# Optimization experiments

Measured on AMD Instinct MI355X. Metric: run time of the kernel, lower is better.

Reference implementation:

```python
import jax, jax.numpy as jnp
import numpy as np

E = 1024   # embed_dim
H = 16     # num_heads
D = E // H # head dim = 64
L = 1024   # query seq len
S = 1024   # key seq len
N = 4      # batch


def _xavier(key, shape):
    fan_in, fan_out = shape[-1], shape[0]
    if len(shape) == 3:  # attn_W [D, D, H]: torch xavier treats dims (d0, d1*h)
        fan_out, fan_in = shape[0], shape[1] * shape[2]
    scale = jnp.sqrt(6.0 / (fan_in + fan_out)).astype(jnp.float32)
    return jax.random.uniform(key, shape, jnp.float32, -scale, scale)


def setup_inputs() -> dict:
    key = jax.random.key(0)
    ks = jax.random.split(key, 8)
    return {
        "Q": jax.random.normal(ks[0], (L, N, E), jnp.float32),
        "K": jax.random.normal(ks[1], (S, N, E), jnp.float32),
        "V": jax.random.normal(ks[2], (S, N, E), jnp.float32),
        "q_w": _xavier(ks[3], (E, E)),
        "k_w": _xavier(ks[4], (E, E)),
        "v_w": _xavier(ks[5], (E, E)),
        "out_w": _xavier(ks[6], (E, E)),
        "in_bias": jnp.zeros((3, E), jnp.float32),
        "out_bias": jnp.zeros((E,), jnp.float32),
        "attn_W": _xavier(ks[7], (D, D, H)),
    }


def reference(Q, K, V, q_w, k_w, v_w, out_w, in_bias, out_bias, attn_W):
    # in-projections: [l,n,e] x [o,e] -> [l,n,o]
    Qp = jnp.einsum('lni,oi->lno', Q, q_w) + in_bias[0]
    Kp = jnp.einsum('sni,oi->sno', K, k_w) + in_bias[1]
    Vp = jnp.einsum('sni,oi->sno', V, v_w) + in_bias[2]
    # split heads as (head_dim D, num_heads H) -- matches torch .view order
    Qh = Qp.reshape(L, N, D, H)
    Kh = Kp.reshape(S, N, D, H)
    Vh = Vp.reshape(S, N, D, H)
    # 'product' attention: per-head bilinear form q^T W_k k
    scores = jnp.einsum('lnok,oik,snik->lsnk', Qh, attn_W, Kh) / jnp.sqrt(jnp.float32(E))
    W = jax.nn.softmax(scores, axis=1)          # softmax over key dim s
    # dropout p=0.0 -> identity
    O = jnp.einsum('lsnk,snik->lnik', W, Vh).reshape(L, N, E)
    out = O @ out_w + out_bias
    # attention map: sum over heads, reshape [L,S,N] -> [N,L,S] (torch .view semantics = reshape)
    Wmap = W.sum(axis=-1).reshape(-1, L, S) / H
    return out, Wmap
```

## Files before the change

kernel.cpp:

```cpp
#include <hip/hip_runtime.h>
#include <cstdint>

typedef __bf16 bf16x8 __attribute__((ext_vector_type(8)));
typedef float f32x4 __attribute__((ext_vector_type(4)));

#define GLOAD_LDS16(gptr, lptr)                                              \
  __builtin_amdgcn_global_load_lds(                                          \
      (const __attribute__((address_space(1))) void*)(gptr),                 \
      (__attribute__((address_space(3))) void*)(lptr), 16, 0, 0)

static const size_t OFF_QW2BF = 0;
static const size_t OFF_KWBF  = 524288;
static const size_t OFF_VWBF  = 1048576;
static const size_t OFF_OWTBF = 1572864;
static const size_t OFF_QB2   = 2097152;
static const size_t OFF_QWBF  = 2098176;
static const size_t OFF_KHBF  = 4195328;
static const size_t OFF_VTBF  = 6292480;
static const size_t OFF_ST    = 8389632;
static const size_t OFF_OBF   = 8520704;
static const size_t OFF_ABF   = 10617856;

__device__ inline unsigned short f2bf(float f) {
  union { float f; unsigned u; } v; v.f = f;
  const unsigned r = v.u + 0x7FFFu + ((v.u >> 16) & 1u);
  return (unsigned short)(r >> 16);
}

__global__ __launch_bounds__(256) void k_qw2(const float* __restrict__ qw,
    const float* __restrict__ attnW, const float* __restrict__ bias0,
    unsigned short* __restrict__ qw2, float* __restrict__ qb2) {
  const int b = blockIdx.x;
  const int k = b >> 6, i = b & 63;
  const int tid = threadIdx.x;
  __shared__ float aw[64];
  if (tid < 64) aw[tid] = attnW[(tid * 64 + i) * 16 + k] * 0.03125f;
  __syncthreads();
  for (int j = tid; j < 1024; j += 256) {
    float acc = 0.f;
#pragma unroll 8
    for (int o = 0; o < 64; ++o) acc = fmaf(qw[(o * 16 + k) * 1024 + j], aw[o], acc);
    qw2[(size_t)b * 1024 + j] = f2bf(acc);
  }
  if (tid == 0) {
    float acc = 0.f;
    for (int o = 0; o < 64; ++o) acc = fmaf(bias0[o * 16 + k], aw[o], acc);
    qb2[b] = acc;
  }
}

__global__ __launch_bounds__(256) void k_cvt2(const float* __restrict__ a,
    const float* __restrict__ b, unsigned short* __restrict__ oa,
    unsigned short* __restrict__ ob) {
  const int o = blockIdx.x;
  const int dst = (o & 15) * 64 + (o >> 4);
  const int j = threadIdx.x;
  const float4 va = ((const float4*)(a + (size_t)o * 1024))[j];
  ushort4 ha; ha.x = f2bf(va.x); ha.y = f2bf(va.y); ha.z = f2bf(va.z); ha.w = f2bf(va.w);
  ((ushort4*)(oa + (size_t)dst * 1024))[j] = ha;
  const float4 vb = ((const float4*)(b + (size_t)o * 1024))[j];
  ushort4 hb; hb.x = f2bf(vb.x); hb.y = f2bf(vb.y); hb.z = f2bf(vb.z); hb.w = f2bf(vb.w);
  ((ushort4*)(ob + (size_t)dst * 1024))[j] = hb;
}

__global__ __launch_bounds__(256) void k_cvtA(const float* __restrict__ Q,
    const float* __restrict__ K, const float* __restrict__ V,
    unsigned short* __restrict__ out) {
  const int b = blockIdx.x;
  const int m = b >> 10;
  const float* src = m == 0 ? Q : (m == 1 ? K : V);
  unsigned short* dst = out + (size_t)m * 4194304;
#pragma unroll
  for (int q = 0; q < 4; ++q) {
    const int idx = (b & 1023) * 1024 + q * 256 + threadIdx.x;
    const float4 v = ((const float4*)src)[idx];
    ushort4 h; h.x = f2bf(v.x); h.y = f2bf(v.y); h.z = f2bf(v.z); h.w = f2bf(v.w);
    ((ushort4*)dst)[idx] = h;
  }
}

__global__ __launch_bounds__(256) void k_tr(const float* __restrict__ w,
    unsigned short* __restrict__ wt) {
  __shared__ float t[64][65];
  const int j0 = blockIdx.y * 64, o0 = blockIdx.x * 64;
  const int tid = threadIdx.x;
  const int r = tid >> 4, c4 = tid & 15;
#pragma unroll
  for (int q = 0; q < 4; ++q) {
    const int row = r + q * 16;
    const float4 v = *(const float4*)&w[(size_t)(j0 + row) * 1024 + o0 + c4 * 4];
    t[row][c4 * 4 + 0] = v.x; t[row][c4 * 4 + 1] = v.y;
    t[row][c4 * 4 + 2] = v.z; t[row][c4 * 4 + 3] = v.w;
  }
  __syncthreads();
#pragma unroll
  for (int q = 0; q < 4; ++q) {
    const int orow = r + q * 16;
    ushort4 h;
    h.x = f2bf(t[c4 * 4 + 0][orow]); h.y = f2bf(t[c4 * 4 + 1][orow]);
    h.z = f2bf(t[c4 * 4 + 2][orow]); h.w = f2bf(t[c4 * 4 + 3][orow]);
    *(ushort4*)&wt[(size_t)(o0 + orow) * 1024 + j0 + c4 * 4] = h;
  }
}

__global__ __launch_bounds__(256) void k_gemm_in(
    const unsigned short* __restrict__ Abf, const unsigned short* __restrict__ Bq,
    const unsigned short* __restrict__ Bk, const unsigned short* __restrict__ Bv,
    const float* __restrict__ bq, const float* __restrict__ bk,
    const float* __restrict__ bv, unsigned short* __restrict__ Cq,
    unsigned short* __restrict__ Ck, unsigned short* __restrict__ Cv) {
  __shared__ unsigned short As[128 * 64];
  __shared__ unsigned short Bs[128 * 64];
  const int id = blockIdx.x;
  const int g  = (id & 7) + ((id >> 6) << 3);
  const int bx = (id >> 3) & 7;
  const int by = g & 31, bz = g >> 5;
  const unsigned short* A = Abf + (size_t)bz * 4194304;
  const unsigned short* B = bz == 0 ? Bq : (bz == 1 ? Bk : Bv);
  const float* bias       = bz == 0 ? bq : (bz == 1 ? bk : bv);
  unsigned short* C       = bz == 0 ? Cq : (bz == 1 ? Ck : Cv);
  const int m0 = by * 128, o0 = bx * 128;
  const int tid = threadIdx.x;
  const int wid = tid >> 6, lane = tid & 63;
  const int wr = wid >> 1, wc = wid & 1;
  const int lr = lane & 15, lk = lane >> 4;
  int srow[4], scol[4];
#pragma unroll
  for (int q = 0; q < 4; ++q) {
    const int idx = q * 256 + tid;
    srow[q] = idx >> 3;
    scol[q] = (((idx & 7) ^ ((idx >> 3) & 7)) << 3);
  }
  f32x4 acc[4][4];
#pragma unroll
  for (int i = 0; i < 4; ++i)
#pragma unroll
    for (int j = 0; j < 4; ++j) acc[i][j] = (f32x4){0.f, 0.f, 0.f, 0.f};

  for (int t = 0; t < 16; ++t) {
    const int kb = t * 64;
#pragma unroll
    for (int q = 0; q < 4; ++q) {
      GLOAD_LDS16(&A[(size_t)(m0 + srow[q]) * 1024 + kb + scol[q]],
                  &As[(q * 256 + tid) * 8]);
      GLOAD_LDS16(&B[(size_t)(o0 + srow[q]) * 1024 + kb + scol[q]],
                  &Bs[(q * 256 + tid) * 8]);
    }
    __syncthreads();
#pragma unroll
    for (int ph = 0; ph < 2; ++ph) {
      const int ck = ph * 4 + lk;
      bf16x8 af[4], bfr[4];
#pragma unroll
      for (int f = 0; f < 4; ++f) {
        const int ra = wr * 64 + f * 16 + lr;
        af[f] = *(const bf16x8*)&As[ra * 64 + ((ck ^ (ra & 7)) << 3)];
        const int rb = wc * 64 + f * 16 + lr;
        bfr[f] = *(const bf16x8*)&Bs[rb * 64 + ((ck ^ (rb & 7)) << 3)];
      }
#pragma unroll
      for (int i = 0; i < 4; ++i)
#pragma unroll
        for (int j = 0; j < 4; ++j)
          acc[i][j] = __builtin_amdgcn_mfma_f32_16x16x32_bf16(af[i], bfr[j], acc[i][j], 0, 0, 0);
    }
    __syncthreads();
  }
#pragma unroll
  for (int fi = 0; fi < 4; ++fi)
#pragma unroll
    for (int fj = 0; fj < 4; ++fj) {
      const int o = o0 + wc * 64 + fj * 16 + lr;
      const int kk = o >> 6, ii = o & 63;
      const float bo = bz == 0 ? bias[o] : bias[ii * 16 + kk];
#pragma unroll
      for (int t = 0; t < 4; ++t) {
        const int m = m0 + wr * 64 + fi * 16 + lk * 4 + t;
        const float v = acc[fi][fj][t] + bo;
        const int l = m >> 2, nn = m & 3;
        if (bz <= 1) {
          C[(((size_t)(nn * 16 + kk) * 1024 + l) << 6) + ii] = f2bf(v);
        } else {
          C[(((size_t)(nn * 16 + kk) * 64 + ii) << 10) + l] = f2bf(v);
        }
      }
    }
}

__global__ __launch_bounds__(256) void k_gemm_out(
    const unsigned short* __restrict__ A, const unsigned short* __restrict__ B,
    const float* __restrict__ bias, float* __restrict__ C) {
  __shared__ unsigned short As[64 * 64];
  __shared__ unsigned short Bs[128 * 64];
  const int id = blockIdx.x;
  const int g  = (id & 7) + ((id >> 6) << 3);
  const int bx = (id >> 3) & 7;
  const int m0 = g * 64, o0 = bx * 128;
  const int tid = threadIdx.x;
  const int wid = tid >> 6, lane = tid & 63;
  const int wr = wid >> 1, wc = wid & 1;
  const int lr = lane & 15, lk = lane >> 4;
  int srow[4], scol[4];
#pragma unroll
  for (int q = 0; q < 4; ++q) {
    const int idx = q * 256 + tid;
    srow[q] = idx >> 3;
    scol[q] = (((idx & 7) ^ ((idx >> 3) & 7)) << 3);
  }
  f32x4 acc[2][4];
#pragma unroll
  for (int i = 0; i < 2; ++i)
#pragma unroll
    for (int j = 0; j < 4; ++j) acc[i][j] = (f32x4){0.f, 0.f, 0.f, 0.f};

  for (int t = 0; t < 16; ++t) {
    const int kb = t * 64;
#pragma unroll
    for (int q = 0; q < 2; ++q)
      GLOAD_LDS16(&A[(size_t)(m0 + srow[q]) * 1024 + kb + scol[q]],
                  &As[(q * 256 + tid) * 8]);
#pragma unroll
    for (int q = 0; q < 4; ++q)
      GLOAD_LDS16(&B[(size_t)(o0 + srow[q]) * 1024 + kb + scol[q]],
                  &Bs[(q * 256 + tid) * 8]);
    __syncthreads();
#pragma unroll
    for (int ph = 0; ph < 2; ++ph) {
      const int ck = ph * 4 + lk;
      bf16x8 af[2], bfr[4];
#pragma unroll
      for (int f = 0; f < 2; ++f) {
        const int ra = wr * 32 + f * 16 + lr;
        af[f] = *(const bf16x8*)&As[ra * 64 + ((ck ^ (ra & 7)) << 3)];
      }
#pragma unroll
      for (int f = 0; f < 4; ++f) {
        const int rb = wc * 64 + f * 16 + lr;
        bfr[f] = *(const bf16x8*)&Bs[rb * 64 + ((ck ^ (rb & 7)) << 3)];
      }
#pragma unroll
      for (int i = 0; i < 2; ++i)
#pragma unroll
        for (int j = 0; j < 4; ++j)
          acc[i][j] = __builtin_amdgcn_mfma_f32_16x16x32_bf16(af[i], bfr[j], acc[i][j], 0, 0, 0);
    }
    __syncthreads();
  }
#pragma unroll
  for (int fi = 0; fi < 2; ++fi)
#pragma unroll
    for (int fj = 0; fj < 4; ++fj) {
      const int o = o0 + wc * 64 + fj * 16 + lr;
      const float bo = bias[o];
#pragma unroll
      for (int t = 0; t < 4; ++t) {
        const int m = m0 + wr * 32 + fi * 16 + lk * 4 + t;
        C[(size_t)m * 1024 + o] = acc[fi][fj][t] + bo;
      }
    }
}

__global__ __launch_bounds__(256) void k_flash(
    const unsigned short* __restrict__ Qbf, const unsigned short* __restrict__ Khbf,
    const unsigned short* __restrict__ Vtbf, float* __restrict__ stats,
    unsigned short* __restrict__ Obf) {
  __shared__ unsigned short Kd[2][64 * 64];
  __shared__ unsigned short Vd[2][64 * 64];
  __shared__ unsigned short Ps[4][16 * 64];
  const int ob = blockIdx.x;
  const int b = (ob & 7) * 128 + (ob >> 3);
  const int lt = b & 15, k = (b >> 4) & 15, n = b >> 8;
  const int l0 = lt * 64;
  const int tid = threadIdx.x, w = tid >> 6, lane = tid & 63;
  const int lr = lane & 15, lk = lane >> 4;
  const size_t hb = (size_t)(n * 16 + k) * 65536;
  const unsigned short* qrow = Qbf + hb + (size_t)(l0 + w * 16 + lr) * 64;
  const bf16x8 qa0 = *(const bf16x8*)(qrow + lk * 8);
  const bf16x8 qa1 = *(const bf16x8*)(qrow + 32 + lk * 8);
  const int swz = lr & 7;
  int srow[2], scol[2];
#pragma unroll
  for (int q = 0; q < 2; ++q) {
    const int idx = q * 256 + tid;
    srow[q] = idx >> 3;
    scol[q] = (((idx & 7) ^ ((idx >> 3) & 7)) << 3);
  }
  const unsigned short* Kb = Khbf + hb;
  const unsigned short* Vb = Vtbf + hb;
  int4 kreg[2], vreg[2];
#pragma unroll
  for (int q = 0; q < 2; ++q) {
    kreg[q] = *(const int4*)(Kb + (size_t)srow[q] * 64 + scol[q]);
    vreg[q] = *(const int4*)(Vb + (size_t)srow[q] * 1024 + scol[q]);
  }
#pragma unroll
  for (int q = 0; q < 2; ++q) {
    *(int4*)&Kd[0][(q * 256 + tid) * 8] = kreg[q];
    *(int4*)&Vd[0][(q * 256 + tid) * 8] = vreg[q];
  }
  float m_ = -1e30f, Z_ = 0.f;
  f32x4 oacc[4];
#pragma unroll
  for (int it = 0; it < 4; ++it) oacc[it] = (f32x4){0.f, 0.f, 0.f, 0.f};
  __syncthreads();

  for (int t0 = 0; t0 < 16; ++t0) {
    const int cur = t0 & 1;
    if (t0 < 15) {
      const int s1 = (t0 + 1) * 64;
#pragma unroll
      for (int q = 0; q < 2; ++q) {
        kreg[q] = *(const int4*)(Kb + (size_t)(s1 + srow[q]) * 64 + scol[q]);
        vreg[q] = *(const int4*)(Vb + (size_t)srow[q] * 1024 + s1 + scol[q]);
      }
    }
    f32x4 sc[4];
#pragma unroll
    for (int st = 0; st < 4; ++st) {
      const int r = st * 16 + lr;
      const bf16x8 kb0 = *(const bf16x8*)&Kd[cur][r * 64 + ((lk ^ (r & 7)) << 3)];
      const bf16x8 kb1 = *(const bf16x8*)&Kd[cur][r * 64 + (((4 + lk) ^ (r & 7)) << 3)];
      f32x4 z = (f32x4){0.f, 0.f, 0.f, 0.f};
      z = __builtin_amdgcn_mfma_f32_16x16x32_bf16(kb0, qa0, z, 0, 0, 0);
      sc[st] = __builtin_amdgcn_mfma_f32_16x16x32_bf16(kb1, qa1, z, 0, 0, 0);
    }
    float tm = fmaxf(fmaxf(fmaxf(sc[0][0], sc[0][1]), fmaxf(sc[0][2], sc[0][3])),
                     fmaxf(fmaxf(sc[1][0], sc[1][1]), fmaxf(sc[1][2], sc[1][3])));
    tm = fmaxf(tm, fmaxf(fmaxf(fmaxf(sc[2][0], sc[2][1]), fmaxf(sc[2][2], sc[2][3])),
                         fmaxf(fmaxf(sc[3][0], sc[3][1]), fmaxf(sc[3][2], sc[3][3]))));
    tm = fmaxf(tm, __shfl_xor(tm, 16));
    tm = fmaxf(tm, __shfl_xor(tm, 32));
    const float mn = fmaxf(m_, tm);
    const float fac = __expf(m_ - mn);
    m_ = mn;
    float rs = 0.f;
    float p[4][4];
#pragma unroll
    for (int st = 0; st < 4; ++st)
#pragma unroll
      for (int t = 0; t < 4; ++t) {
        p[st][t] = __expf(sc[st][t] - mn);
        rs += p[st][t];
      }
    rs += __shfl_xor(rs, 16);
    rs += __shfl_xor(rs, 32);
    Z_ = Z_ * fac + rs;
#pragma unroll
    for (int st = 0; st < 4; ++st) {
      ushort4 pk;
      pk.x = f2bf(p[st][0]); pk.y = f2bf(p[st][1]);
      pk.z = f2bf(p[st][2]); pk.w = f2bf(p[st][3]);
      const int c = (st * 4 + lk) ^ (swz << 1);
      *(ushort4*)&Ps[w][lr * 64 + c * 4] = pk;
    }
    float fr[4];
#pragma unroll
    for (int t = 0; t < 4; ++t) fr[t] = __shfl(fac, lk * 4 + t);
    const f32x4 facv = {fr[0], fr[1], fr[2], fr[3]};
    const bf16x8 pa0 = *(const bf16x8*)&Ps[w][lr * 64 + ((lk ^ swz) << 3)];
    const bf16x8 pa1 = *(const bf16x8*)&Ps[w][lr * 64 + (((4 + lk) ^ swz) << 3)];
#pragma unroll
    for (int it = 0; it < 4; ++it) {
      const int r = it * 16 + lr;
      const bf16x8 bv0 = *(const bf16x8*)&Vd[cur][r * 64 + ((lk ^ (r & 7)) << 3)];
      const bf16x8 bv1 = *(const bf16x8*)&Vd[cur][r * 64 + (((4 + lk) ^ (r & 7)) << 3)];
      f32x4 o = oacc[it] * facv;
      o = __builtin_amdgcn_mfma_f32_16x16x32_bf16(pa0, bv0, o, 0, 0, 0);
      oacc[it] = __builtin_amdgcn_mfma_f32_16x16x32_bf16(pa1, bv1, o, 0, 0, 0);
    }
    if (t0 < 15) {
#pragma unroll
      for (int q = 0; q < 2; ++q) {
        *(int4*)&Kd[cur ^ 1][(q * 256 + tid) * 8] = kreg[q];
        *(int4*)&Vd[cur ^ 1][(q * 256 + tid) * 8] = vreg[q];
      }
    }
    __syncthreads();
  }

  if (lane < 16) {
    const size_t so = ((size_t)(n * 16 + k) * 1024 + l0 + w * 16 + lr) * 2;
    stats[so] = m_;
    stats[so + 1] = Z_;
  }
  const float iz = 1.f / Z_;
  float izr[4];
#pragma unroll
  for (int t = 0; t < 4; ++t) izr[t] = __shfl(iz, lk * 4 + t);
#pragma unroll
  for (int it = 0; it < 4; ++it)
#pragma unroll
    for (int t = 0; t < 4; ++t) {
      const int l = l0 + w * 16 + lk * 4 + t;
      const int i = it * 16 + lr;
      Obf[(size_t)(l * 4 + n) * 1024 + i * 16 + k] = f2bf(oacc[it][t] * izr[t]);
    }
}

__global__ __launch_bounds__(256) void k_wmap(const unsigned short* __restrict__ Qbf,
    const unsigned short* __restrict__ Khbf, const float* __restrict__ stats,
    float* __restrict__ Wmap) {
  __shared__ unsigned short Kst[2][64 * 64];
  const int ob = blockIdx.x;
  const int b = (ob & 7) * 128 + (ob >> 3);
  const int st = b & 15, lt = (b >> 4) & 15, n = b >> 8;
  const int l0 = lt * 64, s0 = st * 64;
  const int tid = threadIdx.x, w = tid >> 6, lane = tid & 63;
  const int lr = lane & 15, lk = lane >> 4;
  int srow[2], scol[2];
#pragma unroll
  for (int q = 0; q < 2; ++q) {
    const int idx = q * 256 + tid;
    srow[q] = idx >> 3;
    scol[q] = (((idx & 7) ^ ((idx >> 3) & 7)) << 3);
  }
  int4 kreg[2];
#pragma unroll
  for (int q = 0; q < 2; ++q)
    kreg[q] = *(const int4*)(Khbf + (size_t)(n * 16) * 65536 +
                             (size_t)(s0 + srow[q]) * 64 + scol[q]);
#pragma unroll
  for (int q = 0; q < 2; ++q)
    *(int4*)&Kst[0][(q * 256 + tid) * 8] = kreg[q];
  f32x4 wsum[4];
#pragma unroll
  for (int i = 0; i < 4; ++i) wsum[i] = (f32x4){0.f, 0.f, 0.f, 0.f};
  __syncthreads();

  for (int k = 0; k < 16; ++k) {
    const int cur = k & 1;
    const size_t hb = (size_t)(n * 16 + k) * 65536;
    if (k < 15) {
      const size_t hb1 = (size_t)(n * 16 + k + 1) * 65536;
#pragma unroll
      for (int q = 0; q < 2; ++q)
        kreg[q] = *(const int4*)(Khbf + hb1 + (size_t)(s0 + srow[q]) * 64 + scol[q]);
    }
    const unsigned short* qrow = Qbf + hb + (size_t)(l0 + w * 16 + lr) * 64;
    const bf16x8 a0 = *(const bf16x8*)(qrow + lk * 8);
    const bf16x8 a1 = *(const bf16x8*)(qrow + 32 + lk * 8);
    float mv[4], izv[4];
#pragma unroll
    for (int t = 0; t < 4; ++t) {
      const float2 mz = *(const float2*)(stats +
          ((size_t)(n * 16 + k) * 1024 + l0 + w * 16 + lk * 4 + t) * 2);
      mv[t] = mz.x; izv[t] = 1.f / mz.y;
    }
#pragma unroll
    for (int st2 = 0; st2 < 4; ++st2) {
      const int r = st2 * 16 + lr;
      const bf16x8 kb0 = *(const bf16x8*)&Kst[cur][r * 64 + ((lk ^ (r & 7)) << 3)];
      const bf16x8 kb1 = *(const bf16x8*)&Kst[cur][r * 64 + (((4 + lk) ^ (r & 7)) << 3)];
      f32x4 z = (f32x4){0.f, 0.f, 0.f, 0.f};
      z = __builtin_amdgcn_mfma_f32_16x16x32_bf16(a0, kb0, z, 0, 0, 0);
      z = __builtin_amdgcn_mfma_f32_16x16x32_bf16(a1, kb1, z, 0, 0, 0);
#pragma unroll
      for (int t = 0; t < 4; ++t)
        wsum[st2][t] += __expf(z[t] - mv[t]) * izv[t];
    }
    if (k < 15) {
#pragma unroll
      for (int q = 0; q < 2; ++q)
        *(int4*)&Kst[cur ^ 1][(q * 256 + tid) * 8] = kreg[q];
    }
    __syncthreads();
  }
#pragma unroll
  for (int st2 = 0; st2 < 4; ++st2)
#pragma unroll
    for (int t = 0; t < 4; ++t) {
      const int l = l0 + w * 16 + lk * 4 + t;
      const int s = s0 + st2 * 16 + lr;
      Wmap[((size_t)l * 1024 + s) * 4 + n] = wsum[st2][t] * 0.0625f;
    }
}

extern "C" void kernel_launch(void* const* d_in, const int* in_sizes, int n_in,
                              void* d_out, int out_size, void* d_ws, size_t ws_size,
                              hipStream_t stream) {
  (void)in_sizes; (void)n_in; (void)out_size; (void)ws_size;
  const float* Q        = (const float*)d_in[0];
  const float* K        = (const float*)d_in[1];
  const float* V        = (const float*)d_in[2];
  const float* q_w      = (const float*)d_in[3];
  const float* k_w      = (const float*)d_in[4];
  const float* v_w      = (const float*)d_in[5];
  const float* out_w    = (const float*)d_in[6];
  const float* in_bias  = (const float*)d_in[7];
  const float* out_bias = (const float*)d_in[8];
  const float* attn_W   = (const float*)d_in[9];
  float* ws = (float*)d_ws;
  unsigned short* qw2bf = (unsigned short*)(ws + OFF_QW2BF);
  unsigned short* kwbf  = (unsigned short*)(ws + OFF_KWBF);
  unsigned short* vwbf  = (unsigned short*)(ws + OFF_VWBF);
  unsigned short* owtbf = (unsigned short*)(ws + OFF_OWTBF);
  float* qb2 = ws + OFF_QB2;
  unsigned short* Qwbf = (unsigned short*)(ws + OFF_QWBF);
  unsigned short* Khbf = (unsigned short*)(ws + OFF_KHBF);
  unsigned short* Vtbf = (unsigned short*)(ws + OFF_VTBF);
  float* st = ws + OFF_ST;
  unsigned short* Obf  = (unsigned short*)(ws + OFF_OBF);
  unsigned short* Abf  = (unsigned short*)(ws + OFF_ABF);
  float* out  = (float*)d_out;
  float* Wmap = out + 4194304;

  k_qw2<<<1024, 256, 0, stream>>>(q_w, attn_W, in_bias, qw2bf, qb2);
  k_cvt2<<<1024, 256, 0, stream>>>(k_w, v_w, kwbf, vwbf);
  k_cvtA<<<3072, 256, 0, stream>>>(Q, K, V, Abf);
  k_tr<<<dim3(16, 16), 256, 0, stream>>>(out_w, owtbf);
  k_gemm_in<<<768, 256, 0, stream>>>(Abf, qw2bf, kwbf, vwbf,
                                     qb2, in_bias + 1024, in_bias + 2048,
                                     Qwbf, Khbf, Vtbf);
  k_flash<<<1024, 256, 0, stream>>>(Qwbf, Khbf, Vtbf, st, Obf);
  k_wmap<<<1024, 256, 0, stream>>>(Qwbf, Khbf, st, Wmap);
  k_gemm_out<<<512, 256, 0, stream>>>(Obf, owtbf, out_bias, out);
}
```

Before: 196.6 us.

## Merge prep kernels into one launch and double-buffer GEMM LDS loads

Four preprocessing kernels (q_w/attn_W fold, weight conversion, input bf16 conversion, out_w transpose) are fused into a single launch that dispatches on block index. This cuts launch overhead and the tail gaps between small kernels. Both projection GEMMs now double-buffer their LDS tiles, issuing async global-to-LDS loads for the next K step before computing the current one. They wait with explicit vmcnt counts and raw s_barrier. LDS usage doubles, which may lower occupancy, and the manual waitcnt values must match the number of outstanding loads.

```diff
diff --git a/kernel.cpp b/kernel.cpp
--- a/kernel.cpp
+++ b/kernel.cpp
@@ -27,79 +27,74 @@
   return (unsigned short)(r >> 16);
 }
 
-__global__ __launch_bounds__(256) void k_qw2(const float* __restrict__ qw,
-    const float* __restrict__ attnW, const float* __restrict__ bias0,
-    unsigned short* __restrict__ qw2, float* __restrict__ qb2) {
+__global__ __launch_bounds__(256) void k_prep(const float* __restrict__ Q,
+    const float* __restrict__ K, const float* __restrict__ V,
+    const float* __restrict__ qw, const float* __restrict__ kw,
+    const float* __restrict__ vw, const float* __restrict__ ow,
+    const float* __restrict__ attnW, const float* __restrict__ in_bias,
+    unsigned short* __restrict__ qw2, float* __restrict__ qb2,
+    unsigned short* __restrict__ kwbf, unsigned short* __restrict__ vwbf,
+    unsigned short* __restrict__ owtbf, unsigned short* __restrict__ Abf) {
+  __shared__ float sh[64 * 65];
   const int b = blockIdx.x;
-  const int k = b >> 6, i = b & 63;
   const int tid = threadIdx.x;
-  __shared__ float aw[64];
-  if (tid < 64) aw[tid] = attnW[(tid * 64 + i) * 16 + k] * 0.03125f;
-  __syncthreads();
-  for (int j = tid; j < 1024; j += 256) {
-    float acc = 0.f;
+  if (b < 1024) {
+    const int k = b >> 6, i = b & 63;
+    if (tid < 64) sh[tid] = attnW[(tid * 64 + i) * 16 + k] * 0.03125f;
+    __syncthreads();
+    for (int j = tid; j < 1024; j += 256) {
+      float acc = 0.f;
 #pragma unroll 8
-    for (int o = 0; o < 64; ++o) acc = fmaf(qw[(o * 16 + k) * 1024 + j], aw[o], acc);
-    qw2[(size_t)b * 1024 + j] = f2bf(acc);
-  }
-  if (tid == 0) {
-    float acc = 0.f;
-    for (int o = 0; o < 64; ++o) acc = fmaf(bias0[o * 16 + k], aw[o], acc);
-    qb2[b] = acc;
-  }
-}
-
-__global__ __launch_bounds__(256) void k_cvt2(const float* __restrict__ a,
-    const float* __restrict__ b, unsigned short* __restrict__ oa,
-    unsigned short* __restrict__ ob) {
-  const int o = blockIdx.x;
-  const int dst = (o & 15) * 64 + (o >> 4);
-  const int j = threadIdx.x;
-  const float4 va = ((const float4*)(a + (size_t)o * 1024))[j];
-  ushort4 ha; ha.x = f2bf(va.x); ha.y = f2bf(va.y); ha.z = f2bf(va.z); ha.w = f2bf(va.w);
-  ((ushort4*)(oa + (size_t)dst * 1024))[j] = ha;
-  const float4 vb = ((const float4*)(b + (size_t)o * 1024))[j];
-  ushort4 hb; hb.x = f2bf(vb.x); hb.y = f2bf(vb.y); hb.z = f2bf(vb.z); hb.w = f2bf(vb.w);
-  ((ushort4*)(ob + (size_t)dst * 1024))[j] = hb;
-}
-
-__global__ __launch_bounds__(256) void k_cvtA(const float* __restrict__ Q,
-    const float* __restrict__ K, const float* __restrict__ V,
-    unsigned short* __restrict__ out) {
-  const int b = blockIdx.x;
-  const int m = b >> 10;
-  const float* src = m == 0 ? Q : (m == 1 ? K : V);
-  unsigned short* dst = out + (size_t)m * 4194304;
-#pragma unroll
-  for (int q = 0; q < 4; ++q) {
-    const int idx = (b & 1023) * 1024 + q * 256 + threadIdx.x;
-    const float4 v = ((const float4*)src)[idx];
-    ushort4 h; h.x = f2bf(v.x); h.y = f2bf(v.y); h.z = f2bf(v.z); h.w = f2bf(v.w);
-    ((ushort4*)dst)[idx] = h;
-  }
-}
-
-__global__ __launch_bounds__(256) void k_tr(const float* __restrict__ w,
-    unsigned short* __restrict__ wt) {
-  __shared__ float t[64][65];
-  const int j0 = blockIdx.y * 64, o0 = blockIdx.x * 64;
-  const int tid = threadIdx.x;
-  const int r = tid >> 4, c4 = tid & 15;
-#pragma unroll
-  for (int q = 0; q < 4; ++q) {
-    const int row = r + q * 16;
-    const float4 v = *(const float4*)&w[(size_t)(j0 + row) * 1024 + o0 + c4 * 4];
-    t[row][c4 * 4 + 0] = v.x; t[row][c4 * 4 + 1] = v.y;
-    t[row][c4 * 4 + 2] = v.z; t[row][c4 * 4 + 3] = v.w;
-  }
-  __syncthreads();
-#pragma unroll
-  for (int q = 0; q < 4; ++q) {
-    const int orow = r + q * 16;
-    ushort4 h;
-    h.x = f2bf(t[c4 * 4 + 0][orow]); h.y = f2bf(t[c4 * 4 + 1][orow]);
-    h.z = f2bf(t[c4 * 4 + 2][orow]); h.w = f2bf(t[c4 * 4 + 3][orow]);
-    *(ushort4*)&wt[(size_t)(o0 + orow) * 1024 + j0 + c4 * 4] = h;
+      for (int o = 0; o < 64; ++o) acc = fmaf(qw[(o * 16 + k) * 1024 + j], sh[o], acc);
+      qw2[(size_t)b * 1024 + j] = f2bf(acc);
+    }
+    if (tid == 0) {
+      float acc = 0.f;
+      for (int o = 0; o < 64; ++o) acc = fmaf(in_bias[o * 16 + k], sh[o], acc);
+      qb2[b] = acc;
+    }
+  } else if (b < 2048) {
+    const int o = b - 1024;
+    const int dst = (o & 15) * 64 + (o >> 4);
+    const float4 va = ((const float4*)(kw + (size_t)o * 1024))[tid];
+    ushort4 ha; ha.x = f2bf(va.x); ha.y = f2bf(va.y); ha.z = f2bf(va.z); ha.w = f2bf(va.w);
+    ((ushort4*)(kwbf + (size_t)dst * 1024))[tid] = ha;
+    const float4 vb = ((const float4*)(vw + (size_t)o * 1024))[tid];
+    ushort4 hb; hb.x = f2bf(vb.x); hb.y = f2bf(vb.y); hb.z = f2bf(vb.z); hb.w = f2bf(vb.w);
+    ((ushort4*)(vwbf + (size_t)dst * 1024))[tid] = hb;
+  } else if (b < 5120) {
+    const int bb = b - 2048;
+    const int m = bb >> 10;
+    const float* src = m == 0 ? Q : (m == 1 ? K : V);
+    unsigned short* dst = Abf + (size_t)m * 4194304;
+#pragma unroll
+    for (int q = 0; q < 4; ++q) {
+      const int idx = (bb & 1023) * 1024 + q * 256 + tid;
+      const float4 v = ((const float4*)src)[idx];
+      ushort4 h; h.x = f2bf(v.x); h.y = f2bf(v.y); h.z = f2bf(v.z); h.w = f2bf(v.w);
+      ((ushort4*)dst)[idx] = h;
+    }
+  } else {
+    float (*t)[65] = (float(*)[65])sh;
+    const int tb = b - 5120;
+    const int o0 = (tb & 15) * 64, j0 = (tb >> 4) * 64;
+    const int r = tid >> 4, c4 = tid & 15;
+#pragma unroll
+    for (int q = 0; q < 4; ++q) {
+      const int row = r + q * 16;
+      const float4 v = *(const float4*)&ow[(size_t)(j0 + row) * 1024 + o0 + c4 * 4];
+      t[row][c4 * 4 + 0] = v.x; t[row][c4 * 4 + 1] = v.y;
+      t[row][c4 * 4 + 2] = v.z; t[row][c4 * 4 + 3] = v.w;
+    }
+    __syncthreads();
+#pragma unroll
+    for (int q = 0; q < 4; ++q) {
+      const int orow = r + q * 16;
+      ushort4 h;
+      h.x = f2bf(t[c4 * 4 + 0][orow]); h.y = f2bf(t[c4 * 4 + 1][orow]);
+      h.z = f2bf(t[c4 * 4 + 2][orow]); h.w = f2bf(t[c4 * 4 + 3][orow]);
+      *(ushort4*)&owtbf[(size_t)(o0 + orow) * 1024 + j0 + c4 * 4] = h;
+    }
   }
 }
 
@@ -109,8 +104,8 @@
     const float* __restrict__ bq, const float* __restrict__ bk,
     const float* __restrict__ bv, unsigned short* __restrict__ Cq,
     unsigned short* __restrict__ Ck, unsigned short* __restrict__ Cv) {
-  __shared__ unsigned short As[128 * 64];
-  __shared__ unsigned short Bs[128 * 64];
+  __shared__ unsigned short As[2][128 * 64];
+  __shared__ unsigned short Bs[2][128 * 64];
   const int id = blockIdx.x;
   const int g  = (id & 7) + ((id >> 6) << 3);
   const int bx = (id >> 3) & 7;
@@ -137,16 +132,28 @@
 #pragma unroll
     for (int j = 0; j < 4; ++j) acc[i][j] = (f32x4){0.f, 0.f, 0.f, 0.f};
 
+#pragma unroll
+  for (int q = 0; q < 4; ++q) {
+    GLOAD_LDS16(&A[(size_t)(m0 + srow[q]) * 1024 + scol[q]], &As[0][(q * 256 + tid) * 8]);
+    GLOAD_LDS16(&B[(size_t)(o0 + srow[q]) * 1024 + scol[q]], &Bs[0][(q * 256 + tid) * 8]);
+  }
+
   for (int t = 0; t < 16; ++t) {
-    const int kb = t * 64;
-#pragma unroll
-    for (int q = 0; q < 4; ++q) {
-      GLOAD_LDS16(&A[(size_t)(m0 + srow[q]) * 1024 + kb + scol[q]],
-                  &As[(q * 256 + tid) * 8]);
-      GLOAD_LDS16(&B[(size_t)(o0 + srow[q]) * 1024 + kb + scol[q]],
-                  &Bs[(q * 256 + tid) * 8]);
-    }
-    __syncthreads();
+    const int cur = t & 1;
+    if (t < 15) {
+      const int kb = (t + 1) * 64;
+#pragma unroll
+      for (int q = 0; q < 4; ++q) {
+        GLOAD_LDS16(&A[(size_t)(m0 + srow[q]) * 1024 + kb + scol[q]],
+                    &As[cur ^ 1][(q * 256 + tid) * 8]);
+        GLOAD_LDS16(&B[(size_t)(o0 + srow[q]) * 1024 + kb + scol[q]],
+                    &Bs[cur ^ 1][(q * 256 + tid) * 8]);
+      }
+      asm volatile("s_waitcnt vmcnt(8)" ::: "memory");
+    } else {
+      asm volatile("s_waitcnt vmcnt(0)" ::: "memory");
+    }
+    __builtin_amdgcn_s_barrier();
 #pragma unroll
     for (int ph = 0; ph < 2; ++ph) {
       const int ck = ph * 4 + lk;
@@ -154,9 +161,9 @@
 #pragma unroll
       for (int f = 0; f < 4; ++f) {
         const int ra = wr * 64 + f * 16 + lr;
-        af[f] = *(const bf16x8*)&As[ra * 64 + ((ck ^ (ra & 7)) << 3)];
+        af[f] = *(const bf16x8*)&As[cur][ra * 64 + ((ck ^ (ra & 7)) << 3)];
         const int rb = wc * 64 + f * 16 + lr;
-        bfr[f] = *(const bf16x8*)&Bs[rb * 64 + ((ck ^ (rb & 7)) << 3)];
+        bfr[f] = *(const bf16x8*)&Bs[cur][rb * 64 + ((ck ^ (rb & 7)) << 3)];
       }
 #pragma unroll
       for (int i = 0; i < 4; ++i)
@@ -164,7 +171,7 @@
         for (int j = 0; j < 4; ++j)
           acc[i][j] = __builtin_amdgcn_mfma_f32_16x16x32_bf16(af[i], bfr[j], acc[i][j], 0, 0, 0);
     }
-    __syncthreads();
+    __builtin_amdgcn_s_barrier();
   }
 #pragma unroll
   for (int fi = 0; fi < 4; ++fi)
@@ -190,8 +197,8 @@
 __global__ __launch_bounds__(256) void k_gemm_out(
     const unsigned short* __restrict__ A, const unsigned short* __restrict__ B,
     const float* __restrict__ bias, float* __restrict__ C) {
-  __shared__ unsigned short As[64 * 64];
-  __shared__ unsigned short Bs[128 * 64];
+  __shared__ unsigned short As[2][64 * 64];
+  __shared__ unsigned short Bs[2][128 * 64];
   const int id = blockIdx.x;
   const int g  = (id & 7) + ((id >> 6) << 3);
   const int bx = (id >> 3) & 7;
@@ -213,17 +220,30 @@
 #pragma unroll
     for (int j = 0; j < 4; ++j) acc[i][j] = (f32x4){0.f, 0.f, 0.f, 0.f};
 
+#pragma unroll
+  for (int q = 0; q < 2; ++q)
+    GLOAD_LDS16(&A[(size_t)(m0 + srow[q]) * 1024 + scol[q]], &As[0][(q * 256 + tid) * 8]);
+#pragma unroll
+  for (int q = 0; q < 4; ++q)
+    GLOAD_LDS16(&B[(size_t)(o0 + srow[q]) * 1024 + scol[q]], &Bs[0][(q * 256 + tid) * 8]);
+
   for (int t = 0; t < 16; ++t) {
-    const int kb = t * 64;
-#pragma unroll
-    for (int q = 0; q < 2; ++q)
-      GLOAD_LDS16(&A[(size_t)(m0 + srow[q]) * 1024 + kb + scol[q]],
-                  &As[(q * 256 + tid) * 8]);
-#pragma unroll
-    for (int q = 0; q < 4; ++q)
-      GLOAD_LDS16(&B[(size_t)(o0 + srow[q]) * 1024 + kb + scol[q]],
-                  &Bs[(q * 256 + tid) * 8]);
-    __syncthreads();
+    const int cur = t & 1;
+    if (t < 15) {
+      const int kb = (t + 1) * 64;
+#pragma unroll
+      for (int q = 0; q < 2; ++q)
+        GLOAD_LDS16(&A[(size_t)(m0 + srow[q]) * 1024 + kb + scol[q]],
+                    &As[cur ^ 1][(q * 256 + tid) * 8]);
+#pragma unroll
+      for (int q = 0; q < 4; ++q)
+        GLOAD_LDS16(&B[(size_t)(o0 + srow[q]) * 1024 + kb + scol[q]],
+                    &Bs[cur ^ 1][(q * 256 + tid) * 8]);
+      asm volatile("s_waitcnt vmcnt(6)" ::: "memory");
+    } else {
+      asm volatile("s_waitcnt vmcnt(0)" ::: "memory");
+    }
+    __builtin_amdgcn_s_barrier();
 #pragma unroll
     for (int ph = 0; ph < 2; ++ph) {
       const int ck = ph * 4 + lk;
@@ -231,12 +251,12 @@
 #pragma unroll
       for (int f = 0; f < 2; ++f) {
         const int ra = wr * 32 + f * 16 + lr;
-        af[f] = *(const bf16x8*)&As[ra * 64 + ((ck ^ (ra & 7)) << 3)];
+        af[f] = *(const bf16x8*)&As[cur][ra * 64 + ((ck ^ (ra & 7)) << 3)];
       }
 #pragma unroll
       for (int f = 0; f < 4; ++f) {
         const int rb = wc * 64 + f * 16 + lr;
-        bfr[f] = *(const bf16x8*)&Bs[rb * 64 + ((ck ^ (rb & 7)) << 3)];
+        bfr[f] = *(const bf16x8*)&Bs[cur][rb * 64 + ((ck ^ (rb & 7)) << 3)];
       }
 #pragma unroll
       for (int i = 0; i < 2; ++i)
@@ -244,7 +264,7 @@
         for (int j = 0; j < 4; ++j)
           acc[i][j] = __builtin_amdgcn_mfma_f32_16x16x32_bf16(af[i], bfr[j], acc[i][j], 0, 0, 0);
     }
-    __syncthreads();
+    __builtin_amdgcn_s_barrier();
   }
 #pragma unroll
   for (int fi = 0; fi < 2; ++fi)
@@ -504,10 +524,8 @@
   float* out  = (float*)d_out;
   float* Wmap = out + 4194304;
 
-  k_qw2<<<1024, 256, 0, stream>>>(q_w, attn_W, in_bias, qw2bf, qb2);
-  k_cvt2<<<1024, 256, 0, stream>>>(k_w, v_w, kwbf, vwbf);
-  k_cvtA<<<3072, 256, 0, stream>>>(Q, K, V, Abf);
-  k_tr<<<dim3(16, 16), 256, 0, stream>>>(out_w, owtbf);
+  k_prep<<<5376, 256, 0, stream>>>(Q, K, V, q_w, k_w, v_w, out_w, attn_W,
+                                   in_bias, qw2bf, qb2, kwbf, vwbf, owtbf, Abf);
   k_gemm_in<<<768, 256, 0, stream>>>(Abf, qw2bf, kwbf, vwbf,
                                      qb2, in_bias + 1024, in_bias + 2048,
                                      Qwbf, Khbf, Vtbf);
```

Measured after the change: 181.4 us. 7.7% less time.
